# Kernel optimization log

Hardware: AMD Instinct MI355X
Metric: run time of the kernel (lower is better)

Reference implementation:

```python
import jax, jax.numpy as jnp
import numpy as np

B, S, D = 2, 2048, 4096
NH, NKV = 32, 8
HD = D // NH          # 128
NREP = NH // NKV      # 4 (GQA groups)


def _rope(t, cos, sin):
    # t: [b, s, h, d]; cos/sin: [s, d//2]; interleaved (real, imag) pairs on last dim
    tr = t.reshape(*t.shape[:-1], -1, 2)
    a, b = tr[..., 0], tr[..., 1]
    c = cos[None, :, None, :]
    s = sin[None, :, None, :]
    out = jnp.stack([a * c - b * s, a * s + b * c], axis=-1)
    return out.reshape(t.shape)


def _repeat_kv(t, n_rep):
    # [b, s, n_kv, d] -> [b, s, n_kv*n_rep, d]
    b, s, nkv, d = t.shape
    return jnp.broadcast_to(t[:, :, :, None, :], (b, s, nkv, n_rep, d)).reshape(b, s, nkv * n_rep, d)


def setup_inputs() -> dict:
    key = jax.random.key(0)
    ks = jax.random.split(key, 5)
    x = jax.random.normal(ks[0], (B, S, D), jnp.float32)
    wq = jax.random.normal(ks[1], (D, NH * HD), jnp.float32) * 0.02
    wk = jax.random.normal(ks[2], (D, NKV * HD), jnp.float32) * 0.02
    wv = jax.random.normal(ks[3], (D, NKV * HD), jnp.float32) * 0.02
    wo = jax.random.normal(ks[4], (NH * HD, D), jnp.float32) * 0.02
    inv_freq = 1.0 / (10000.0 ** (jnp.arange(0, HD, 2, dtype=jnp.float32) / HD))
    angles = jnp.arange(S, dtype=jnp.float32)[:, None] * inv_freq[None, :]  # [S, HD//2]
    return {
        "x": x, "wq": wq, "wk": wk, "wv": wv, "wo": wo,
        "freqs_cos": jnp.cos(angles), "freqs_sin": jnp.sin(angles),
        "start_pos": 0,
    }


def reference(x, wq, wk, wv, wo, freqs_cos, freqs_sin, start_pos):
    b, s, _ = x.shape
    xq = (x @ wq).reshape(b, s, NH, HD)
    xk = (x @ wk).reshape(b, s, NKV, HD)
    xv = (x @ wv).reshape(b, s, NKV, HD)
    xq = _rope(xq, freqs_cos, freqs_sin)
    xk = _rope(xk, freqs_cos, freqs_sin)
    # prefill (start_pos=0): cache[:b, :s] = xk/xv, then keys/values read back equal xk/xv
    keys = _repeat_kv(xk, NREP)    # [b, s, NH, HD]
    values = _repeat_kv(xv, NREP)  # [b, s, NH, HD]
    scores = jnp.einsum("bqhd,bkhd->bhqk", xq, keys) / jnp.sqrt(jnp.float32(HD))
    probs = jax.nn.softmax(scores, axis=-1)
    out = jnp.einsum("bhqk,bkhd->bqhd", probs, values).reshape(b, s, NH * HD)
    return out @ wo
```

## Files before the change

### kernel.cpp

```cpp
#include <hip/hip_runtime.h>
#include <hip/hip_bf16.h>
#include <cstdint>

#define B_   2
#define S_   2048
#define D_   4096
#define NH_  32
#define NKV_ 8
#define HD_  128
#define BS_  (B_*S_)
#define NQK_ 6144

typedef __bf16 bf16_t;
typedef __bf16 bf16x8 __attribute__((ext_vector_type(8)));
typedef __bf16 bf16x4 __attribute__((ext_vector_type(4)));
typedef __bf16 bf16x2 __attribute__((ext_vector_type(2)));
typedef float  f32x4  __attribute__((ext_vector_type(4)));

typedef const __attribute__((address_space(1))) void* gas_ptr;
typedef __attribute__((address_space(3))) void* las_ptr;

__device__ __forceinline__ void gload_lds16(const void* g, void* l) {
  __builtin_amdgcn_global_load_lds((gas_ptr)g, (las_ptr)l, 16, 0, 0);
}

#define LD8(p) (*(const bf16x8*)(p))
#define MFMA(a, b, c) __builtin_amdgcn_mfma_f32_16x16x32_bf16(a, b, c, 0, 0, 0)

__global__ __launch_bounds__(256) void k_cvt(const float4* __restrict__ in,
                                             bf16x4* __restrict__ out, int n4) {
  int i = blockIdx.x * 256 + threadIdx.x;
  if (i >= n4) return;
  float4 v = in[i];
  bf16x4 o = { (bf16_t)v.x, (bf16_t)v.y, (bf16_t)v.z, (bf16_t)v.w };
  out[i] = o;
}

__global__ __launch_bounds__(256) void k_transpose_cvt(const float* __restrict__ w,
                                                       bf16_t* __restrict__ wt,
                                                       int K, int N) {
  __shared__ float tile[32][33];
  int n0 = blockIdx.x * 32, k0 = blockIdx.y * 32;
  int tx = threadIdx.x, ty = threadIdx.y;
#pragma unroll
  for (int i = 0; i < 4; i++)
    tile[ty + 8*i][tx] = w[(size_t)(k0 + ty + 8*i) * N + n0 + tx];
  __syncthreads();
#pragma unroll
  for (int i = 0; i < 4; i++)
    wt[(size_t)(n0 + ty + 8*i) * K + k0 + tx] = (bf16_t)tile[tx][ty + 8*i];
}

template <typename CT, int NF>
__global__ __launch_bounds__(512, 2) void k_gemm8p(const bf16_t* __restrict__ A,
                                                   const bf16_t* __restrict__ Bt,
                                                   CT* __restrict__ C,
                                                   int M, int N, int K) {
  __shared__ __align__(16) bf16_t As[2][256 * 64];
  __shared__ __align__(16) bf16_t Bs[2][NF * 64 * 64];
  const int tid = threadIdx.x;
  const int l = tid & 63, w = tid >> 6;
  const int lr = l & 15, lg = l >> 4;
  const int wm = w >> 2, wn = w & 3;

  const int bm = blockIdx.x, bn = blockIdx.y;

  const bf16_t* Ab = A  + (size_t)bm * 256 * K;
  const bf16_t* Bb = Bt + (size_t)bn * (NF * 64) * K;

  int st_row[4], st_col[4], st_dst[4];
#pragma unroll
  for (int j = 0; j < 4; j++) {
    int o = (j * 512 + tid) * 16;
    int row = o >> 7, cb = o & 127;
    st_row[j] = row;
    st_col[j] = (cb ^ ((row & 7) << 4)) >> 1;
    st_dst[j] = o >> 1;
  }

  int aoff[8], boff[NF];
#pragma unroll
  for (int m = 0; m < 8; m++) {
    int r = wm * 128 + m * 16 + lr;
    aoff[m] = r * 64 + (((lg * 16) ^ ((r & 7) << 4)) >> 1);
  }
#pragma unroll
  for (int n = 0; n < NF; n++) {
    int r = wn * (16 * NF) + n * 16 + lr;
    boff[n] = r * 64 + (((lg * 16) ^ ((r & 7) << 4)) >> 1);
  }

  f32x4 acc[8][NF];
#pragma unroll
  for (int m = 0; m < 8; m++)
#pragma unroll
    for (int n = 0; n < NF; n++) acc[m][n] = f32x4{0.f, 0.f, 0.f, 0.f};

  auto stageA = [&](int k, int h) {
    const int kt = k << 6;
    const int rof = h << 7;
#pragma unroll
    for (int j = 0; j < 2; j++)
      gload_lds16(Ab + (size_t)(st_row[j] + rof) * K + kt + st_col[j],
                  &As[k & 1][0] + (rof << 6) + st_dst[j]);
  };
  auto stageB = [&](int k) {
    const int kt = k << 6;
#pragma unroll
    for (int j = 0; j < NF; j++)
      gload_lds16(Bb + (size_t)st_row[j] * K + kt + st_col[j],
                  &Bs[k & 1][0] + st_dst[j]);
  };

  const int NT = K >> 6;
  stageA(0, 0); stageA(0, 1); stageB(0); stageB(1);
  if constexpr (NF == 3) asm volatile("s_waitcnt vmcnt(3)" ::: "memory");
  else                   asm volatile("s_waitcnt vmcnt(4)" ::: "memory");
  __builtin_amdgcn_s_barrier();

  for (int k = 0; k < NT; ++k) {
    const bf16_t* Ap = &As[k & 1][0];
    const bf16_t* Bp = &Bs[k & 1][0];
    const bool s1 = (k + 1 < NT), s2 = (k + 2 < NT);
    bf16x8 bfr[NF], a[4];

#pragma unroll
    for (int n = 0; n < NF; n++) bfr[n] = LD8(Bp + boff[n]);
#pragma unroll
    for (int m = 0; m < 4; m++) a[m] = LD8(Ap + aoff[m]);
    if (s1) stageA(k + 1, 0);
    __builtin_amdgcn_s_barrier();
    asm volatile("s_waitcnt lgkmcnt(0)" ::: "memory");
    __builtin_amdgcn_s_setprio(1);
#pragma unroll
    for (int m = 0; m < 4; m++)
#pragma unroll
      for (int n = 0; n < NF; n++)
        acc[m][n] = MFMA(a[m], bfr[n], acc[m][n]);
    __builtin_amdgcn_s_setprio(0);
    __builtin_amdgcn_s_barrier();

#pragma unroll
    for (int m = 0; m < 4; m++) a[m] = LD8(Ap + aoff[m + 4]);
    if (s1) stageA(k + 1, 1);
    __builtin_amdgcn_s_barrier();
    asm volatile("s_waitcnt lgkmcnt(0)" ::: "memory");
    __builtin_amdgcn_s_setprio(1);
#pragma unroll
    for (int m = 0; m < 4; m++)
#pragma unroll
      for (int n = 0; n < NF; n++)
        acc[m + 4][n] = MFMA(a[m], bfr[n], acc[m + 4][n]);
    __builtin_amdgcn_s_setprio(0);
    __builtin_amdgcn_s_barrier();

#pragma unroll
    for (int n = 0; n < NF; n++) bfr[n] = LD8(Bp + (boff[n] ^ 32));
#pragma unroll
    for (int m = 0; m < 4; m++) a[m] = LD8(Ap + (aoff[m] ^ 32));
    __builtin_amdgcn_s_barrier();
    asm volatile("s_waitcnt lgkmcnt(0)" ::: "memory");
    __builtin_amdgcn_s_setprio(1);
#pragma unroll
    for (int m = 0; m < 4; m++)
#pragma unroll
      for (int n = 0; n < NF; n++)
        acc[m][n] = MFMA(a[m], bfr[n], acc[m][n]);
    __builtin_amdgcn_s_setprio(0);
    __builtin_amdgcn_s_barrier();

#pragma unroll
    for (int m = 0; m < 4; m++) a[m] = LD8(Ap + (aoff[m + 4] ^ 32));
    if (s2) {
      stageB(k + 2);
      if constexpr (NF == 3) asm volatile("s_waitcnt vmcnt(3)" ::: "memory");
      else                   asm volatile("s_waitcnt vmcnt(4)" ::: "memory");
    } else if (s1) {
      asm volatile("s_waitcnt vmcnt(0)" ::: "memory");
    }
    __builtin_amdgcn_s_barrier();
    asm volatile("s_waitcnt lgkmcnt(0)" ::: "memory");
    __builtin_amdgcn_s_setprio(1);
#pragma unroll
    for (int m = 0; m < 4; m++)
#pragma unroll
      for (int n = 0; n < NF; n++)
        acc[m + 4][n] = MFMA(a[m], bfr[n], acc[m + 4][n]);
    __builtin_amdgcn_s_setprio(0);
    __builtin_amdgcn_s_barrier();
  }

#pragma unroll
  for (int m = 0; m < 8; m++) {
    int row0 = bm * 256 + wm * 128 + m * 16 + lg * 4;
#pragma unroll
    for (int n = 0; n < NF; n++) {
      int col = bn * (NF * 64) + wn * (16 * NF) + n * 16 + lr;
#pragma unroll
      for (int i = 0; i < 4; i++)
        C[(size_t)(row0 + i) * N + col] = (CT)acc[m][n][i];
    }
  }
}

__global__ __launch_bounds__(256) void k_rope(const bf16_t* __restrict__ qkv,
                                              const float* __restrict__ fcos,
                                              const float* __restrict__ fsin,
                                              bf16_t* __restrict__ dst,
                                              int nheads, int col_off, float mul) {
  int idx = blockIdx.x * 256 + threadIdx.x;
  int p = idx & 63;
  int h = (idx >> 6) % nheads;
  int bs = idx / (64 * nheads);
  int s = bs & (S_ - 1);
  int b = bs >> 11;
  const bf16_t* src = qkv + (size_t)bs * NQK_ + col_off + h * HD_ + 2 * p;
  bf16x2 ab = *(const bf16x2*)src;
  float a = (float)ab[0], bb = (float)ab[1];
  float c = fcos[s * 64 + p], sn = fsin[s * 64 + p];
  bf16x2 o = { (bf16_t)((a * c - bb * sn) * mul), (bf16_t)((a * sn + bb * c) * mul) };
  *(bf16x2*)(dst + ((((size_t)b * nheads + h) * S_ + s) * HD_) + 2 * p) = o;
}

__global__ __launch_bounds__(256) void k_vtrans(const bf16_t* __restrict__ qkv,
                                                bf16_t* __restrict__ vtr) {
  __shared__ bf16_t tile[32][33];
  int s0 = blockIdx.x * 32, d0 = blockIdx.y * 32, z = blockIdx.z;
  int b = z >> 3, kvh = z & 7;
  int tx = threadIdx.x, ty = threadIdx.y;
#pragma unroll
  for (int i = 0; i < 4; i++)
    tile[ty + 8*i][tx] =
        qkv[(size_t)(b * S_ + s0 + ty + 8*i) * NQK_ + (D_ + NKV_ * HD_) + kvh * HD_ + d0 + tx];
  __syncthreads();
#pragma unroll
  for (int i = 0; i < 4; i++)
    vtr[((size_t)z * HD_ + d0 + ty + 8*i) * S_ + s0 + tx] = tile[tx][ty + 8*i];
}

#define KVBLK 64
__global__ __launch_bounds__(256, 2) void k_flash(const bf16_t* __restrict__ qr,
                                                  const bf16_t* __restrict__ kr,
                                                  const bf16_t* __restrict__ vt,
                                                  bf16_t* __restrict__ ctx) {
  __shared__ __align__(16) bf16_t Ks[2][KVBLK * HD_];
  __shared__ __align__(16) bf16_t Vs[2][HD_ * KVBLK];
  __shared__ __align__(16) char  plds[4][2048];
  const int tid = threadIdx.x;
  const int l = tid & 63, w = tid >> 6;
  const int lr = l & 15, lg = l >> 4;
  const int qb = blockIdx.x, h = blockIdx.y, b = blockIdx.z;
  const int kvh = h >> 2;

  const bf16_t* qbase = qr + (((size_t)b * NH_ + h) * S_ + qb * 128 + w * 32) * HD_;
  const bf16_t* kbase = kr + (((size_t)b * NKV_ + kvh) * S_) * HD_;
  const bf16_t* vbase = vt + (((size_t)b * NKV_ + kvh) * HD_) * S_;

  bf16x8 qf[2][4];
#pragma unroll
  for (int m = 0; m < 2; m++)
#pragma unroll
    for (int kk = 0; kk < 4; kk++)
      qf[m][kk] = *(const bf16x8*)(qbase + (m * 16 + lr) * HD_ + kk * 32 + lg * 8);

  f32x4 o[2][8];
#pragma unroll
  for (int m = 0; m < 2; m++)
#pragma unroll
    for (int n = 0; n < 8; n++) o[m][n] = f32x4{0.f, 0.f, 0.f, 0.f};
  float mR[2][4], lR[2][4];
#pragma unroll
  for (int m = 0; m < 2; m++)
#pragma unroll
    for (int i = 0; i < 4; i++) { mR[m][i] = -1e30f; lR[m][i] = 0.f; }

  auto stage = [&](int bu, int t) {
    const int kb = t * KVBLK;
#pragma unroll
    for (int j = 0; j < 4; j++) {
      int o_ = (tid + 256 * j) * 16;
      int row = o_ >> 8, cb = o_ & 255;
      int scb = cb ^ ((row & 7) << 4);
      gload_lds16(kbase + (size_t)(kb + row) * HD_ + (scb >> 1),
                  &Ks[bu][0] + (o_ >> 1));
    }
#pragma unroll
    for (int j = 0; j < 4; j++) {
      int o_ = (tid + 256 * j) * 16;
      int row = o_ >> 7, cb = o_ & 127;
      int scb = cb ^ ((row & 7) << 4);
      gload_lds16(vbase + (size_t)row * S_ + kb + (scb >> 1),
                  &Vs[bu][0] + (o_ >> 1));
    }
  };

  const int nt = S_ / KVBLK;
  stage(0, 0);
  __syncthreads();
  int buf = 0;

  for (int t = 0; t < nt; t++) {
    if (t + 1 < nt) stage(buf ^ 1, t + 1);
    const bf16_t* Kb = &Ks[buf][0];
    const bf16_t* Vb = &Vs[buf][0];

    f32x4 sc[2][4];
#pragma unroll
    for (int m = 0; m < 2; m++)
#pragma unroll
      for (int n = 0; n < 4; n++) sc[m][n] = f32x4{0.f, 0.f, 0.f, 0.f};
    __builtin_amdgcn_s_setprio(1);
#pragma unroll
    for (int n = 0; n < 4; n++) {
#pragma unroll
      for (int kk = 0; kk < 4; kk++) {
        int r = n * 16 + lr;
        int cb = (kk * 64 + lg * 16) ^ ((r & 7) << 4);
        bf16x8 kf = *(const bf16x8*)(Kb + (((r << 8) + cb) >> 1));
        sc[0][n] = MFMA(qf[0][kk], kf, sc[0][n]);
        sc[1][n] = MFMA(qf[1][kk], kf, sc[1][n]);
      }
    }
    __builtin_amdgcn_s_setprio(0);

    bf16x8 pf[2][2];
#pragma unroll
    for (int m = 0; m < 2; m++) {
      float tmax[4];
#pragma unroll
      for (int i = 0; i < 4; i++) {
        float tmx = fmaxf(fmaxf(sc[m][0][i], sc[m][1][i]),
                          fmaxf(sc[m][2][i], sc[m][3][i]));
        tmx = fmaxf(tmx, __shfl_xor(tmx, 1));
        tmx = fmaxf(tmx, __shfl_xor(tmx, 2));
        tmx = fmaxf(tmx, __shfl_xor(tmx, 4));
        tmx = fmaxf(tmx, __shfl_xor(tmx, 8));
        tmax[i] = tmx;
      }
      float need = tmax[0] - mR[m][0];
#pragma unroll
      for (int i = 1; i < 4; i++) need = fmaxf(need, tmax[i] - mR[m][i]);
      if (!__all(need <= 8.0f)) {
        float alpha[4];
#pragma unroll
        for (int i = 0; i < 4; i++) {
          float mnew = fmaxf(mR[m][i], tmax[i]);
          alpha[i] = __expf(mR[m][i] - mnew);
          mR[m][i] = mnew;
          lR[m][i] *= alpha[i];
        }
#pragma unroll
        for (int n = 0; n < 8; n++)
#pragma unroll
          for (int i = 0; i < 4; i++) o[m][n][i] *= alpha[i];
      }
      float psum[4] = {0.f, 0.f, 0.f, 0.f};
#pragma unroll
      for (int n = 0; n < 4; n++)
#pragma unroll
        for (int i = 0; i < 4; i++) {
          float pv = __expf(sc[m][n][i] - mR[m][i]);
          psum[i] += pv;
          int r = lg * 4 + i;
          int cbyte = (n * 32 + lr * 2) ^ ((r & 7) << 4);
          *(bf16_t*)(&plds[w][r * 128 + cbyte]) = (bf16_t)pv;
        }
#pragma unroll
      for (int i = 0; i < 4; i++) {
        float t2 = psum[i];
        t2 += __shfl_xor(t2, 1);
        t2 += __shfl_xor(t2, 2);
        t2 += __shfl_xor(t2, 4);
        t2 += __shfl_xor(t2, 8);
        lR[m][i] += t2;
      }
      pf[m][0] = *(const bf16x8*)(&plds[w][lr * 128 + ((lg * 16) ^ ((lr & 7) << 4))]);
      pf[m][1] = *(const bf16x8*)(&plds[w][lr * 128 + ((64 + lg * 16) ^ ((lr & 7) << 4))]);
    }

    __builtin_amdgcn_s_setprio(1);
#pragma unroll
    for (int n = 0; n < 8; n++) {
#pragma unroll
      for (int kk = 0; kk < 2; kk++) {
        int r = n * 16 + lr;
        int cb = (kk * 64 + lg * 16) ^ ((r & 7) << 4);
        bf16x8 vf = *(const bf16x8*)(Vb + (((r << 7) + cb) >> 1));
        o[0][n] = MFMA(pf[0][kk], vf, o[0][n]);
        o[1][n] = MFMA(pf[1][kk], vf, o[1][n]);
      }
    }
    __builtin_amdgcn_s_setprio(0);
    __syncthreads();
    buf ^= 1;
  }

#pragma unroll
  for (int m = 0; m < 2; m++)
#pragma unroll
    for (int n = 0; n < 8; n++)
#pragma unroll
      for (int i = 0; i < 4; i++) {
        int srow = qb * 128 + w * 32 + m * 16 + lg * 4 + i;
        int d = n * 16 + lr;
        ctx[((size_t)(b * S_ + srow)) * D_ + h * HD_ + d] = (bf16_t)(o[m][n][i] / lR[m][i]);
      }
}

extern "C" void kernel_launch(void* const* d_in, const int* in_sizes, int n_in,
                              void* d_out, int out_size, void* d_ws, size_t ws_size,
                              hipStream_t stream) {
  const float* x    = (const float*)d_in[0];
  const float* wq   = (const float*)d_in[1];
  const float* wk   = (const float*)d_in[2];
  const float* wv   = (const float*)d_in[3];
  const float* wo   = (const float*)d_in[4];
  const float* fcos = (const float*)d_in[5];
  const float* fsin = (const float*)d_in[6];
  float* out = (float*)d_out;

  const size_t SZ_XB    = (size_t)BS_ * D_ * 2;
  const size_t SZ_WQKVT = (size_t)NQK_ * D_ * 2;
  const size_t SZ_WOT   = (size_t)D_ * D_ * 2;
  char* p = (char*)d_ws;
  bf16_t* xb    = (bf16_t*)p;
  bf16_t* wqkvt = (bf16_t*)(p + SZ_XB);
  bf16_t* wot   = (bf16_t*)(p + SZ_XB + SZ_WQKVT);
  bf16_t* qkv   = (bf16_t*)(p + SZ_XB + SZ_WQKVT + SZ_WOT);
  bf16_t* qrope = xb;
  bf16_t* krope = wqkvt;
  bf16_t* vtr   = wqkvt + (size_t)BS_ * NKV_ * HD_;
  bf16_t* ctx   = qkv;

  dim3 tb(32, 8);
  k_cvt<<<BS_ * D_ / 1024, 256, 0, stream>>>((const float4*)x, (bf16x4*)xb, BS_ * D_ / 4);
  k_transpose_cvt<<<dim3(D_ / 32, D_ / 32), tb, 0, stream>>>(wq, wqkvt, D_, D_);
  k_transpose_cvt<<<dim3(32, D_ / 32), tb, 0, stream>>>(wk, wqkvt + (size_t)D_ * D_, D_, NKV_ * HD_);
  k_transpose_cvt<<<dim3(32, D_ / 32), tb, 0, stream>>>(wv, wqkvt + (size_t)(D_ + NKV_ * HD_) * D_, D_, NKV_ * HD_);
  k_transpose_cvt<<<dim3(D_ / 32, D_ / 32), tb, 0, stream>>>(wo, wot, D_, D_);
  k_gemm8p<bf16_t, 3><<<dim3(BS_ / 256, NQK_ / 192), 512, 0, stream>>>(xb, wqkvt, qkv, BS_, NQK_, D_);
  k_rope<<<BS_ * NH_ * 64 / 256, 256, 0, stream>>>(qkv, fcos, fsin, qrope, NH_, 0, 0.08838834764831845f);
  k_rope<<<BS_ * NKV_ * 64 / 256, 256, 0, stream>>>(qkv, fcos, fsin, krope, NKV_, D_, 1.0f);
  k_vtrans<<<dim3(S_ / 32, HD_ / 32, B_ * NKV_), tb, 0, stream>>>(qkv, vtr);
  k_flash<<<dim3(S_ / 128, NH_, B_), 256, 0, stream>>>(qrope, krope, vtr, ctx);
  k_gemm8p<float, 4><<<dim3(BS_ / 256, D_ / 256), 512, 0, stream>>>(ctx, wot, out, BS_, D_, D_);
}
```

Measured before the change: 675.2 us.

## Use exp2 softmax, lazy max reduction, and MFMA row-sum in flash attention

```diff
diff --git a/kernel.cpp b/kernel.cpp
--- a/kernel.cpp
+++ b/kernel.cpp
@@ -22,6 +22,12 @@
 
 __device__ __forceinline__ void gload_lds16(const void* g, void* l) {
   __builtin_amdgcn_global_load_lds((gas_ptr)g, (las_ptr)l, 16, 0, 0);
+}
+
+__device__ __forceinline__ float exp2_fast(float x) {
+  float r;
+  asm("v_exp_f32 %0, %1" : "=v"(r) : "v"(x));
+  return r;
 }
 
 #define LD8(p) (*(const bf16x8*)(p))
@@ -239,6 +245,7 @@
 }
 
 #define KVBLK 64
+#define SM_THR 12.0f
 __global__ __launch_bounds__(256, 2) void k_flash(const bf16_t* __restrict__ qr,
                                                   const bf16_t* __restrict__ kr,
                                                   const bf16_t* __restrict__ vt,
@@ -263,16 +270,20 @@
     for (int kk = 0; kk < 4; kk++)
       qf[m][kk] = *(const bf16x8*)(qbase + (m * 16 + lr) * HD_ + kk * 32 + lg * 8);
 
-  f32x4 o[2][8];
+  bf16x8 ones;
+#pragma unroll
+  for (int j = 0; j < 8; j++) ones[j] = (bf16_t)1.0f;
+
+  f32x4 o[2][9];
 #pragma unroll
   for (int m = 0; m < 2; m++)
 #pragma unroll
-    for (int n = 0; n < 8; n++) o[m][n] = f32x4{0.f, 0.f, 0.f, 0.f};
-  float mR[2][4], lR[2][4];
+    for (int n = 0; n < 9; n++) o[m][n] = f32x4{0.f, 0.f, 0.f, 0.f};
+  float mR[2][4];
 #pragma unroll
   for (int m = 0; m < 2; m++)
 #pragma unroll
-    for (int i = 0; i < 4; i++) { mR[m][i] = -1e30f; lR[m][i] = 0.f; }
+    for (int i = 0; i < 4; i++) mR[m][i] = -1e30f;
 
   auto stage = [&](int bu, int t) {
     const int kb = t * KVBLK;
@@ -326,54 +337,38 @@
     bf16x8 pf[2][2];
 #pragma unroll
     for (int m = 0; m < 2; m++) {
-      float tmax[4];
+      float chk = -1e30f;
 #pragma unroll
       for (int i = 0; i < 4; i++) {
-        float tmx = fmaxf(fmaxf(sc[m][0][i], sc[m][1][i]),
-                          fmaxf(sc[m][2][i], sc[m][3][i]));
-        tmx = fmaxf(tmx, __shfl_xor(tmx, 1));
-        tmx = fmaxf(tmx, __shfl_xor(tmx, 2));
-        tmx = fmaxf(tmx, __shfl_xor(tmx, 4));
-        tmx = fmaxf(tmx, __shfl_xor(tmx, 8));
-        tmax[i] = tmx;
+        float lm = fmaxf(fmaxf(sc[m][0][i], sc[m][1][i]),
+                         fmaxf(sc[m][2][i], sc[m][3][i]));
+        chk = fmaxf(chk, lm - mR[m][i]);
       }
-      float need = tmax[0] - mR[m][0];
-#pragma unroll
-      for (int i = 1; i < 4; i++) need = fmaxf(need, tmax[i] - mR[m][i]);
-      if (!__all(need <= 8.0f)) {
-        float alpha[4];
+      if (!__all(chk <= SM_THR)) {
 #pragma unroll
         for (int i = 0; i < 4; i++) {
-          float mnew = fmaxf(mR[m][i], tmax[i]);
-          alpha[i] = __expf(mR[m][i] - mnew);
+          float tmx = fmaxf(fmaxf(sc[m][0][i], sc[m][1][i]),
+                            fmaxf(sc[m][2][i], sc[m][3][i]));
+          tmx = fmaxf(tmx, __shfl_xor(tmx, 1));
+          tmx = fmaxf(tmx, __shfl_xor(tmx, 2));
+          tmx = fmaxf(tmx, __shfl_xor(tmx, 4));
+          tmx = fmaxf(tmx, __shfl_xor(tmx, 8));
+          float mnew = fmaxf(mR[m][i], tmx);
+          float alpha = exp2_fast(mR[m][i] - mnew);
           mR[m][i] = mnew;
-          lR[m][i] *= alpha[i];
+#pragma unroll
+          for (int n = 0; n < 9; n++) o[m][n][i] *= alpha;
         }
-#pragma unroll
-        for (int n = 0; n < 8; n++)
-#pragma unroll
-          for (int i = 0; i < 4; i++) o[m][n][i] *= alpha[i];
       }
-      float psum[4] = {0.f, 0.f, 0.f, 0.f};
 #pragma unroll
       for (int n = 0; n < 4; n++)
 #pragma unroll
         for (int i = 0; i < 4; i++) {
-          float pv = __expf(sc[m][n][i] - mR[m][i]);
-          psum[i] += pv;
+          float pv = exp2_fast(sc[m][n][i] - mR[m][i]);
           int r = lg * 4 + i;
           int cbyte = (n * 32 + lr * 2) ^ ((r & 7) << 4);
           *(bf16_t*)(&plds[w][r * 128 + cbyte]) = (bf16_t)pv;
         }
-#pragma unroll
-      for (int i = 0; i < 4; i++) {
-        float t2 = psum[i];
-        t2 += __shfl_xor(t2, 1);
-        t2 += __shfl_xor(t2, 2);
-        t2 += __shfl_xor(t2, 4);
-        t2 += __shfl_xor(t2, 8);
-        lR[m][i] += t2;
-      }
       pf[m][0] = *(const bf16x8*)(&plds[w][lr * 128 + ((lg * 16) ^ ((lr & 7) << 4))]);
       pf[m][1] = *(const bf16x8*)(&plds[w][lr * 128 + ((64 + lg * 16) ^ ((lr & 7) << 4))]);
     }
@@ -390,6 +385,10 @@
         o[1][n] = MFMA(pf[1][kk], vf, o[1][n]);
       }
     }
+    o[0][8] = MFMA(pf[0][0], ones, o[0][8]);
+    o[0][8] = MFMA(pf[0][1], ones, o[0][8]);
+    o[1][8] = MFMA(pf[1][0], ones, o[1][8]);
+    o[1][8] = MFMA(pf[1][1], ones, o[1][8]);
     __builtin_amdgcn_s_setprio(0);
     __syncthreads();
     buf ^= 1;
@@ -398,13 +397,15 @@
 #pragma unroll
   for (int m = 0; m < 2; m++)
 #pragma unroll
-    for (int n = 0; n < 8; n++)
-#pragma unroll
-      for (int i = 0; i < 4; i++) {
-        int srow = qb * 128 + w * 32 + m * 16 + lg * 4 + i;
+    for (int i = 0; i < 4; i++) {
+      float inv = 1.0f / o[m][8][i];
+      int srow = qb * 128 + w * 32 + m * 16 + lg * 4 + i;
+#pragma unroll
+      for (int n = 0; n < 8; n++) {
         int d = n * 16 + lr;
-        ctx[((size_t)(b * S_ + srow)) * D_ + h * HD_ + d] = (bf16_t)(o[m][n][i] / lR[m][i]);
+        ctx[((size_t)(b * S_ + srow)) * D_ + h * HD_ + d] = (bf16_t)(o[m][n][i] * inv);
       }
+    }
 }
 
 extern "C" void kernel_launch(void* const* d_in, const int* in_sizes, int n_in,
@@ -432,6 +433,8 @@
   bf16_t* vtr   = wqkvt + (size_t)BS_ * NKV_ * HD_;
   bf16_t* ctx   = qkv;
 
+  const float QSCALE = (float)(0.08838834764831845 * 1.4426950408889634);
+
   dim3 tb(32, 8);
   k_cvt<<<BS_ * D_ / 1024, 256, 0, stream>>>((const float4*)x, (bf16x4*)xb, BS_ * D_ / 4);
   k_transpose_cvt<<<dim3(D_ / 32, D_ / 32), tb, 0, stream>>>(wq, wqkvt, D_, D_);
@@ -439,7 +442,7 @@
   k_transpose_cvt<<<dim3(32, D_ / 32), tb, 0, stream>>>(wv, wqkvt + (size_t)(D_ + NKV_ * HD_) * D_, D_, NKV_ * HD_);
   k_transpose_cvt<<<dim3(D_ / 32, D_ / 32), tb, 0, stream>>>(wo, wot, D_, D_);
   k_gemm8p<bf16_t, 3><<<dim3(BS_ / 256, NQK_ / 192), 512, 0, stream>>>(xb, wqkvt, qkv, BS_, NQK_, D_);
-  k_rope<<<BS_ * NH_ * 64 / 256, 256, 0, stream>>>(qkv, fcos, fsin, qrope, NH_, 0, 0.08838834764831845f);
+  k_rope<<<BS_ * NH_ * 64 / 256, 256, 0, stream>>>(qkv, fcos, fsin, qrope, NH_, 0, QSCALE);
   k_rope<<<BS_ * NKV_ * 64 / 256, 256, 0, stream>>>(qkv, fcos, fsin, krope, NKV_, D_, 1.0f);
   k_vtrans<<<dim3(S_ / 32, HD_ / 32, B_ * NKV_), tb, 0, stream>>>(qkv, vtr);
   k_flash<<<dim3(S_ / 128, NH_, B_), 256, 0, stream>>>(qrope, krope, vtr, ctx);
```

Result: faster. 606.7 us (-10.2%).
